# Performance work log

Measured on AMD Instinct MI355X. Metric: run time of the kernel, lower is better.

The kernel has to match this reference:

```python
import jax, jax.numpy as jnp
import numpy as np

D_MODEL = 1024
N_HEADS = 16
D_K = D_MODEL // N_HEADS
SEQ = 2048
BATCH = 2
THETA = 10000.0


def apply_rope(x, positions, theta):
    # x: [..., h, s, d_k], positions: [s]
    d_k = x.shape[-1]
    inv_freq = 1.0 / (theta ** (jnp.arange(0, d_k, 2, dtype=jnp.float32) / d_k))  # [d_k/2]
    ang = positions.astype(jnp.float32)[:, None] * inv_freq[None, :]  # [s, d_k/2]
    cos, sin = jnp.cos(ang), jnp.sin(ang)
    xe, xo = x[..., 0::2], x[..., 1::2]
    re = xe * cos - xo * sin
    ro = xe * sin + xo * cos
    return jnp.stack([re, ro], axis=-1).reshape(x.shape)


def setup_inputs() -> dict:
    key = jax.random.key(0)
    ks = jax.random.split(key, 7)
    f = lambda k, s: jax.random.normal(k, s, dtype=jnp.float32)
    return {
        "Q": f(ks[0], (BATCH, SEQ, D_MODEL)),
        "K": f(ks[1], (BATCH, SEQ, D_MODEL)),
        "V": f(ks[2], (BATCH, SEQ, D_MODEL)),
        "w_q": f(ks[3], (D_MODEL, D_MODEL)) * 0.02,
        "w_k": f(ks[4], (D_MODEL, D_MODEL)) * 0.02,
        "w_v": f(ks[5], (D_MODEL, D_MODEL)) * 0.02,
        "w_o": f(ks[6], (D_MODEL, D_MODEL)) * 0.02,
        "mask": jnp.tril(jnp.ones((SEQ, SEQ), dtype=bool)),
        "token_positions": jnp.arange(SEQ, dtype=jnp.int32),
    }


def reference(Q, K, V, w_q, w_k, w_v, w_o, mask, token_positions):
    h, d_k = N_HEADS, D_K
    # projections: weight is [h*d_k, d_model], applied as x @ W^T
    def proj(x, w):
        y = jnp.einsum('bsd,ed->bse', x, w)
        b, s, _ = y.shape
        return y.reshape(b, s, h, d_k).transpose(0, 2, 1, 3)  # [b,h,s,d_k]
    q = proj(Q, w_q)
    k = proj(K, w_k)
    v = proj(V, w_v)
    q = apply_rope(q, token_positions, THETA)
    k = apply_rope(k, token_positions, THETA)
    scores = jnp.einsum('bhqd,bhkd->bhqk', q, k) / jnp.sqrt(jnp.float32(d_k))
    scores = jnp.where(mask, scores, -jnp.inf)
    attn = jax.nn.softmax(scores, axis=-1)
    out = jnp.einsum('bhqk,bhkd->bhqd', attn, v)
    b, _, s, _ = out.shape
    out = out.transpose(0, 2, 1, 3).reshape(b, s, h * d_k)
    return jnp.einsum('bse,de->bsd', out, w_o)
```

## Files before the change

### kernel.cpp

```cpp
#include <hip/hip_runtime.h>

#define SEQ 2048
#define BATCH 2
#define DM 1024
#define NH 16
#define DK 64
#define BH (BATCH*NH)

typedef __attribute__((ext_vector_type(8))) short bf16x8;
typedef __attribute__((ext_vector_type(4))) float f32x4;

__device__ __forceinline__ ushort f2bf(float f) {
  union { float f; unsigned u; } v; v.f = f;
  unsigned r = (v.u + 0x7fffu + ((v.u >> 16) & 1u)) >> 16;
  return (ushort)r;
}
__device__ __forceinline__ float bf2f(ushort h) {
  union { unsigned u; float f; } v; v.u = ((unsigned)h) << 16;
  return v.f;
}
__device__ __forceinline__ unsigned cvtpk(float lo, float hi) {
  unsigned r;
  asm("v_cvt_pk_bf16_f32 %0, %1, %2" : "=v"(r) : "v"(lo), "v"(hi));
  return r;
}

struct P4 { const float* p0; const float* p1; const float* p2; const float* p3; };
__global__ void k_castN(P4 in, ushort* __restrict__ out, int n4) {
  const float* src = (blockIdx.z == 0) ? in.p0 : (blockIdx.z == 1) ? in.p1
                    : (blockIdx.z == 2) ? in.p2 : in.p3;
  ushort* dst = out + (size_t)blockIdx.z * (size_t)n4 * 4;
  int i = blockIdx.x * blockDim.x + threadIdx.x;
  int st = gridDim.x * blockDim.x;
  for (; i < n4; i += st) {
    float4 v = reinterpret_cast<const float4*>(src)[i];
    ushort4 o;
    o.x = f2bf(v.x); o.y = f2bf(v.y); o.z = f2bf(v.z); o.w = f2bf(v.w);
    reinterpret_cast<ushort4*>(dst)[i] = o;
  }
}

__global__ void k_rope_tab(float* __restrict__ tab) {
  int id = blockIdx.x * blockDim.x + threadIdx.x;
  if (id >= SEQ * 32) return;
  int s = id >> 5, i = id & 31;
  float inv = powf(10000.f, -(float)i / 32.f);
  float ang = (float)s * inv;
  float sn, cs;
  sincosf(ang, &sn, &cs);
  tab[id * 2] = cs;
  tab[id * 2 + 1] = sn;
}

__global__ __launch_bounds__(256) void k_tr_v(const ushort* __restrict__ Y,
                                              ushort* __restrict__ VT) {
  __shared__ ushort tile[64][65];
  const int st = blockIdx.x, bh = blockIdx.y;
  const int b = bh >> 4, h = bh & 15;
  const int d = threadIdx.x & 63, s4 = threadIdx.x >> 6;
#pragma unroll
  for (int p = 0; p < 16; ++p) {
    int sl = p * 4 + s4;
    tile[d][sl] = Y[(size_t)(b * SEQ + st * 64 + sl) * DM + h * 64 + d];
  }
  __syncthreads();
  const int sl = threadIdx.x & 63, d4 = threadIdx.x >> 6;
#pragma unroll
  for (int p = 0; p < 16; ++p) {
    int dl = p * 4 + d4;
    VT[(size_t)bh * DK * SEQ + (size_t)dl * SEQ + st * 64 + sl] = tile[dl][sl];
  }
}

__device__ __forceinline__ void gll16(const void* g, void* l) {
  __builtin_amdgcn_global_load_lds((const __attribute__((address_space(1))) void*)g,
                                   (__attribute__((address_space(3))) void*)l, 16, 0, 0);
}

#define GSTAGE(AD, BD, kk_) do {                                               \
    gll16(A + (size_t)(m0 + w * 16 + lrow) * K + (kk_) + lcol, (void*)((AD) + w * 512));        \
    gll16(A + (size_t)(m0 + 64 + w * 16 + lrow) * K + (kk_) + lcol, (void*)((AD) + 2048 + w * 512)); \
    gll16(Bw + (size_t)(n0 + w * 16 + lrow) * K + (kk_) + lcol, (void*)((BD) + w * 512));       \
    gll16(Bw + (size_t)(n0 + 64 + w * 16 + lrow) * K + (kk_) + lcol, (void*)((BD) + 2048 + w * 512)); \
  } while (0)

#define GCOMP(AS_, BS_) do {                                                   \
    bf16x8 af[4], bfr[4];                                                      \
    _Pragma("unroll")                                                          \
    for (int i = 0; i < 4; ++i)                                                \
      af[i] = *(const bf16x8*)((AS_) + (wr * 64 + i * 16 + l15) * 32 + l4 * 8);\
    _Pragma("unroll")                                                          \
    for (int i = 0; i < 4; ++i)                                                \
      bfr[i] = *(const bf16x8*)((BS_) + (wc * 64 + i * 16 + l15) * 32 + l4 * 8);\
    _Pragma("unroll")                                                          \
    for (int mi = 0; mi < 4; ++mi)                                             \
      _Pragma("unroll")                                                        \
      for (int ni = 0; ni < 4; ++ni)                                           \
        acc[mi][ni] = __builtin_amdgcn_mfma_f32_16x16x32_bf16(af[mi], bfr[ni], acc[mi][ni], 0, 0, 0); \
  } while (0)

__global__ __launch_bounds__(256) void k_gemm_qkv(const ushort* __restrict__ A,
                                                  const ushort* __restrict__ Bw,
                                                  ushort* __restrict__ qT,
                                                  ushort* __restrict__ kT,
                                                  ushort* __restrict__ YV,
                                                  const float* __restrict__ tab,
                                                  float qscale, int M, int N, int K) {
  const int z = blockIdx.z;
  A += (size_t)z * ((size_t)M * K);
  Bw += (size_t)z * ((size_t)N * K);
  __shared__ ushort As0[128 * 32], Bs0[128 * 32];
  __shared__ ushort As1[128 * 32], Bs1[128 * 32];
  const int tid = threadIdx.x;
  const int w = tid >> 6, lane = tid & 63;
  const int l15 = lane & 15, l4 = lane >> 4;
  const int m0 = blockIdx.y * 128, n0 = blockIdx.x * 128;
  const int wr = w >> 1, wc = w & 1;
  const int lrow = lane >> 2, lcol = (lane & 3) * 8;
  f32x4 acc[4][4] = {};
  GSTAGE(As0, Bs0, 0);
  __syncthreads();
  for (int kk = 0; kk < K; kk += 64) {
    GSTAGE(As1, Bs1, kk + 32);
    GCOMP(As0, Bs0);
    __syncthreads();
    if (kk + 64 < K) GSTAGE(As0, Bs0, kk + 64);
    GCOMP(As1, Bs1);
    __syncthreads();
  }
  if (z == 2) {
#pragma unroll
    for (int mi = 0; mi < 4; ++mi)
#pragma unroll
      for (int ni = 0; ni < 4; ++ni)
#pragma unroll
        for (int r = 0; r < 4; ++r) {
          int row = m0 + wr * 64 + mi * 16 + l4 * 4 + r;
          int col = n0 + wc * 64 + ni * 16 + l15;
          YV[(size_t)row * N + col] = f2bf(acc[mi][ni][r]);
        }
  } else {
    const float scale = (z == 0) ? qscale : 1.0f;
    ushort* T = (z == 0) ? qT : kT;
    const bool odd = (l15 & 1);
#pragma unroll
    for (int mi = 0; mi < 4; ++mi)
#pragma unroll
      for (int ni = 0; ni < 4; ++ni)
#pragma unroll
        for (int r = 0; r < 4; ++r) {
          int row = m0 + wr * 64 + mi * 16 + l4 * 4 + r;
          int col = n0 + wc * 64 + ni * 16 + l15;
          float v = acc[mi][ni][r];
          float pv = __shfl_xor(v, 1);
          int s = row & (SEQ - 1);
          int d = col & 63;
          float2 cs = *(const float2*)(tab + ((size_t)s * 32 + (d >> 1)) * 2);
          float xe = odd ? pv : v, xo = odd ? v : pv;
          float outv = (odd ? (xe * cs.y + xo * cs.x) : (xe * cs.x - xo * cs.y)) * scale;
          int bh = (row >> 11) * 16 + (col >> 6);
          T[((size_t)bh * SEQ + s) * 64 + d] = f2bf(outv);
        }
  }
}

#define FSTAGE(AD, BD, kk_) do {                                               \
    gll16(A + (size_t)(m0 + srow) * K + (kk_) + scol, (void*)((AD) + w * 512));\
    gll16(Bw + (size_t)(n0 + srow) * K + (kk_) + scol, (void*)((BD) + w * 512));\
    gll16(Bw + (size_t)(n0 + 64 + srow) * K + (kk_) + scol, (void*)((BD) + 2048 + w * 512)); \
  } while (0)

#define FCOMP(AS_, BS_) do {                                                   \
    bf16x8 af[2], bfr[4];                                                      \
    _Pragma("unroll")                                                          \
    for (int i = 0; i < 2; ++i)                                                \
      af[i] = *(const bf16x8*)((AS_) + (wr * 32 + i * 16 + l15) * 32 + l4 * 8);\
    _Pragma("unroll")                                                          \
    for (int i = 0; i < 4; ++i)                                                \
      bfr[i] = *(const bf16x8*)((BS_) + (wc * 64 + i * 16 + l15) * 32 + l4 * 8);\
    _Pragma("unroll")                                                          \
    for (int mi = 0; mi < 2; ++mi)                                             \
      _Pragma("unroll")                                                        \
      for (int ni = 0; ni < 4; ++ni)                                           \
        acc[mi][ni] = __builtin_amdgcn_mfma_f32_16x16x32_bf16(af[mi], bfr[ni], acc[mi][ni], 0, 0, 0); \
  } while (0)

__global__ __launch_bounds__(256) void k_gemm_f(const ushort* __restrict__ A,
                                                const ushort* __restrict__ Bw,
                                                float* __restrict__ C, int M, int N, int K) {
  __shared__ ushort As0[64 * 32], Bs0[128 * 32];
  __shared__ ushort As1[64 * 32], Bs1[128 * 32];
  const int tid = threadIdx.x;
  const int w = tid >> 6, lane = tid & 63;
  const int l15 = lane & 15, l4 = lane >> 4;
  const int m0 = blockIdx.y * 64, n0 = blockIdx.x * 128;
  const int wr = w >> 1, wc = w & 1;
  const int srow = tid >> 2, scol = (tid & 3) * 8;
  f32x4 acc[2][4] = {};
  FSTAGE(As0, Bs0, 0);
  __syncthreads();
  for (int kk = 0; kk < K; kk += 64) {
    FSTAGE(As1, Bs1, kk + 32);
    FCOMP(As0, Bs0);
    __syncthreads();
    if (kk + 64 < K) FSTAGE(As0, Bs0, kk + 64);
    FCOMP(As1, Bs1);
    __syncthreads();
  }
#pragma unroll
  for (int mi = 0; mi < 2; ++mi)
#pragma unroll
    for (int ni = 0; ni < 4; ++ni)
#pragma unroll
      for (int r = 0; r < 4; ++r) {
        int row = m0 + wr * 32 + mi * 16 + l4 * 4 + r;
        int col = n0 + wc * 64 + ni * 16 + l15;
        C[(size_t)row * N + col] = acc[mi][ni][r];
      }
}

#define STAGE1(DST, src, srcstride) do {                                       \
    _Pragma("unroll")                                                          \
    for (int i_ = 0; i_ < 2; ++i_) {                                           \
      int tt_ = i_ * 256 + tid;                                                \
      int row_ = tt_ >> 3, c_ = (tt_ & 7) ^ (row_ & 7);                        \
      gll16(src + (size_t)row_ * (srcstride) + c_ * 8,                         \
            (void*)((char*)(DST) + (i_ * 256 + w * 64) * 16));                 \
    }                                                                          \
  } while (0)

#define STAGE(KD, VD, kt_) do {                                                \
    const ushort* kb_ = kT + hb + (size_t)(kt_) * 4096;                        \
    const ushort* vb_ = vT + vbase + (size_t)(kt_) * 64;                       \
    STAGE1(KD, kb_, 64);                                                       \
    STAGE1(VD, vb_, SEQ);                                                      \
  } while (0)

#define LDSFRAG(BASE, row_, cidx)                                              \
  (*(const bf16x8*)((const char*)(BASE) + (row_) * 128 + (((cidx) ^ (l15 & 7)) * 16)))

#define SMAXUPD(P, MRUN, LRUN, SO) do {                                        \
    float a0 = fmaxf(fmaxf(P[0][0], P[0][1]), fmaxf(P[0][2], P[0][3]));        \
    float a1 = fmaxf(fmaxf(P[1][0], P[1][1]), fmaxf(P[1][2], P[1][3]));        \
    float a2 = fmaxf(fmaxf(P[2][0], P[2][1]), fmaxf(P[2][2], P[2][3]));        \
    float a3 = fmaxf(fmaxf(P[3][0], P[3][1]), fmaxf(P[3][2], P[3][3]));        \
    float mx = fmaxf(fmaxf(a0, a1), fmaxf(a2, a3));                            \
    mx = fmaxf(mx, __shfl_xor(mx, 16));                                        \
    mx = fmaxf(mx, __shfl_xor(mx, 32));                                        \
    const float mn = fmaxf(MRUN, mx);                                          \
    SO = __builtin_amdgcn_exp2f(MRUN - mn);                                    \
    float rs = 0.f;                                                            \
    _Pragma("unroll")                                                          \
    for (int nf = 0; nf < 4; ++nf) {                                           \
      float e0 = __builtin_amdgcn_exp2f(P[nf][0] - mn);                        \
      float e1 = __builtin_amdgcn_exp2f(P[nf][1] - mn);                        \
      float e2 = __builtin_amdgcn_exp2f(P[nf][2] - mn);                        \
      float e3 = __builtin_amdgcn_exp2f(P[nf][3] - mn);                        \
      P[nf][0] = e0; P[nf][1] = e1; P[nf][2] = e2; P[nf][3] = e3;              \
      rs += (e0 + e1) + (e2 + e3);                                             \
    }                                                                          \
    rs += __shfl_xor(rs, 16);                                                  \
    rs += __shfl_xor(rs, 32);                                                  \
    LRUN = LRUN * SO + rs;                                                     \
    MRUN = mn;                                                                 \
  } while (0)

#define RESCALE(ACC, SO) do {                                                  \
    float soq[4];                                                              \
    _Pragma("unroll")                                                          \
    for (int r = 0; r < 4; ++r) soq[r] = __shfl(SO, l4 * 4 + r);               \
    _Pragma("unroll")                                                          \
    for (int df = 0; df < 4; ++df)                                             \
      _Pragma("unroll")                                                        \
      for (int r = 0; r < 4; ++r) ACC[df][r] *= soq[r];                        \
  } while (0)

#define PWRITE(P, MYP) do {                                                    \
    _Pragma("unroll")                                                          \
    for (int nf = 0; nf < 4; ++nf) {                                           \
      uint2 pk;                                                                \
      pk.x = cvtpk(P[nf][0], P[nf][1]);                                        \
      pk.y = cvtpk(P[nf][2], P[nf][3]);                                        \
      *(uint2*)((MYP) + ((l15 * 128 + nf * 32 + l4 * 8) ^ swz)) = pk;          \
    }                                                                          \
  } while (0)

#define STEP2(KC, VC, KN, VN, kt_, M0, M1, PREF) do {                          \
    if (PREF) { STAGE(KN, VN, (kt_) + 1); }                                    \
    float p0[4][4], p1[4][4];                                                  \
    _Pragma("unroll")                                                          \
    for (int nf = 0; nf < 4; ++nf) {                                           \
      bf16x8 k0_ = LDSFRAG(KC, nf * 16 + l15, l4);                             \
      bf16x8 k1_ = LDSFRAG(KC, nf * 16 + l15, l4 + 4);                         \
      if (M0 >= 0) {                                                           \
        f32x4 z = {0.f, 0.f, 0.f, 0.f};                                        \
        z = __builtin_amdgcn_mfma_f32_16x16x32_bf16(k0_, qb00, z, 0, 0, 0);    \
        z = __builtin_amdgcn_mfma_f32_16x16x32_bf16(k1_, qb01, z, 0, 0, 0);    \
        _Pragma("unroll")                                                      \
        for (int r = 0; r < 4; ++r) {                                          \
          float sc = z[r];                                                     \
          if (M0 == 1 && (nf * 16 + l4 * 4 + r) > (w * 16 + l15)) sc = -INFINITY; \
          p0[nf][r] = sc;                                                      \
        }                                                                      \
      }                                                                        \
      {                                                                        \
        f32x4 z = {0.f, 0.f, 0.f, 0.f};                                        \
        z = __builtin_amdgcn_mfma_f32_16x16x32_bf16(k0_, qb10, z, 0, 0, 0);    \
        z = __builtin_amdgcn_mfma_f32_16x16x32_bf16(k1_, qb11, z, 0, 0, 0);    \
        _Pragma("unroll")                                                      \
        for (int r = 0; r < 4; ++r) {                                          \
          float sc = z[r];                                                     \
          if (M1 == 1 && (nf * 16 + l4 * 4 + r) > (w * 16 + l15)) sc = -INFINITY; \
          p1[nf][r] = sc;                                                      \
        }                                                                      \
      }                                                                        \
    }                                                                          \
    float so0_, so1_;                                                          \
    if (M0 >= 0) { SMAXUPD(p0, mrun0, lrun0, so0_); RESCALE(acc0, so0_); PWRITE(p0, myP0); } \
    SMAXUPD(p1, mrun1, lrun1, so1_); RESCALE(acc1, so1_); PWRITE(p1, myP1);    \
    bf16x8 pa00, pa01, pa10, pa11;                                             \
    if (M0 >= 0) {                                                             \
      pa00 = *(const bf16x8*)(myP0 + ((l15 * 128 + l4 * 16) ^ swz));           \
      pa01 = *(const bf16x8*)(myP0 + ((l15 * 128 + 64 + l4 * 16) ^ swz));      \
    }                                                                          \
    pa10 = *(const bf16x8*)(myP1 + ((l15 * 128 + l4 * 16) ^ swz));             \
    pa11 = *(const bf16x8*)(myP1 + ((l15 * 128 + 64 + l4 * 16) ^ swz));        \
    _Pragma("unroll")                                                          \
    for (int df = 0; df < 4; ++df) {                                           \
      bf16x8 v0_ = LDSFRAG(VC, df * 16 + l15, l4);                             \
      bf16x8 v1_ = LDSFRAG(VC, df * 16 + l15, l4 + 4);                         \
      if (M0 >= 0) {                                                           \
        acc0[df] = __builtin_amdgcn_mfma_f32_16x16x32_bf16(pa00, v0_, acc0[df], 0, 0, 0); \
        acc0[df] = __builtin_amdgcn_mfma_f32_16x16x32_bf16(pa01, v1_, acc0[df], 0, 0, 0); \
      }                                                                        \
      acc1[df] = __builtin_amdgcn_mfma_f32_16x16x32_bf16(pa10, v0_, acc1[df], 0, 0, 0); \
      acc1[df] = __builtin_amdgcn_mfma_f32_16x16x32_bf16(pa11, v1_, acc1[df], 0, 0, 0); \
    }                                                                          \
    __syncthreads();                                                           \
  } while (0)

__global__ __launch_bounds__(256, 3) void k_flash(const ushort* __restrict__ qT,
                                                  const ushort* __restrict__ kT,
                                                  const ushort* __restrict__ vT,
                                                  ushort* __restrict__ AO) {
  __shared__ ushort Ks[2][64 * 64];
  __shared__ ushort Vs[2][64 * 64];
  __shared__ char Plds[4 * 4096];
  const int l = blockIdx.x;
  const int bh = (l & 7) * 4 + ((l >> 3) & 3);
  const int qt = (SEQ / 128 - 1) - (l >> 5);
  const int tid = threadIdx.x, w = tid >> 6, lane = tid & 63;
  const int l15 = lane & 15, l4 = lane >> 4;
  const size_t hb = (size_t)bh * SEQ * DK;
  const size_t vbase = (size_t)bh * DK * SEQ;
  const int qrow0 = qt * 128 + w * 16;
  const int qrow1 = qrow0 + 64;
  const bf16x8 qb00 = *(const bf16x8*)(qT + hb + (size_t)(qrow0 + l15) * 64 + l4 * 8);
  const bf16x8 qb01 = *(const bf16x8*)(qT + hb + (size_t)(qrow0 + l15) * 64 + 32 + l4 * 8);
  const bf16x8 qb10 = *(const bf16x8*)(qT + hb + (size_t)(qrow1 + l15) * 64 + l4 * 8);
  const bf16x8 qb11 = *(const bf16x8*)(qT + hb + (size_t)(qrow1 + l15) * 64 + 32 + l4 * 8);
  f32x4 acc0[4] = {}, acc1[4] = {};
  float mrun0 = -INFINITY, lrun0 = 0.f, mrun1 = -INFINITY, lrun1 = 0.f;
  char* myP0 = (char*)Plds + w * 4096;
  char* myP1 = myP0 + 2048;
  const int swz = (l15 & 7) << 4;
  ushort* kc = &Ks[0][0]; ushort* vc = &Vs[0][0];
  ushort* kn = &Ks[1][0]; ushort* vn = &Vs[1][0];
  STAGE(kc, vc, 0);
  __syncthreads();
  for (int kt = 0; kt < 2 * qt; ++kt) {
    STEP2(kc, vc, kn, vn, kt, 0, 0, true);
    ushort* t;
    t = kc; kc = kn; kn = t;
    t = vc; vc = vn; vn = t;
  }
  STEP2(kc, vc, kn, vn, 2 * qt, 1, 0, true);
  {
    ushort* t;
    t = kc; kc = kn; kn = t;
    t = vc; vc = vn; vn = t;
  }
  STEP2(kc, vc, kn, vn, 2 * qt + 1, -1, 1, false);
  const int b = bh >> 4, h = bh & 15;
  float lq0[4], lq1[4];
#pragma unroll
  for (int r = 0; r < 4; ++r) {
    lq0[r] = __shfl(lrun0, l4 * 4 + r);
    lq1[r] = __shfl(lrun1, l4 * 4 + r);
  }
#pragma unroll
  for (int r = 0; r < 4; ++r) {
    float inv0 = 1.f / lq0[r], inv1 = 1.f / lq1[r];
    int qr0 = qrow0 + l4 * 4 + r, qr1 = qrow1 + l4 * 4 + r;
#pragma unroll
    for (int df = 0; df < 4; ++df) {
      AO[(size_t)(b * SEQ + qr0) * DM + h * 64 + df * 16 + l15] = f2bf(acc0[df][r] * inv0);
      AO[(size_t)(b * SEQ + qr1) * DM + h * 64 + df * 16 + l15] = f2bf(acc1[df][r] * inv1);
    }
  }
}

extern "C" void kernel_launch(void* const* d_in, const int* in_sizes, int n_in,
                              void* d_out, int out_size, void* d_ws, size_t ws_size,
                              hipStream_t stream) {
  const float* Q = (const float*)d_in[0];
  const float* K = (const float*)d_in[1];
  const float* V = (const float*)d_in[2];
  const float* wq = (const float*)d_in[3];
  const float* wk = (const float*)d_in[4];
  const float* wv = (const float*)d_in[5];
  const float* wo = (const float*)d_in[6];
  float* out = (float*)d_out;
  char* ws = (char*)d_ws;

  ushort* XQ = (ushort*)(ws + 0);
  ushort* XK = (ushort*)(ws + 8388608);
  ushort* WQ = (ushort*)(ws + 25165824);
  ushort* qT = (ushort*)(ws + 33554432);
  ushort* kT = (ushort*)(ws + 41943040);
  ushort* YV = (ushort*)(ws + 50331648);
  float* TAB = (float*)(ws + 58720256);
  ushort* vT = XQ;
  ushort* AO = XK;

  const int NX4 = BATCH * SEQ * DM / 4;
  const int NW4 = DM * DM / 4;
  P4 xin = {Q, K, V, nullptr};
  P4 win = {wq, wk, wv, wo};
  k_castN<<<dim3(1024, 1, 3), 256, 0, stream>>>(xin, XQ, NX4);
  k_castN<<<dim3(1024, 1, 4), 256, 0, stream>>>(win, WQ, NW4);
  k_rope_tab<<<(SEQ * 32) / 256, 256, 0, stream>>>(TAB);

  const float QSCALE = 0.125f * 1.4426950408889634f;
  k_gemm_qkv<<<dim3(DM / 128, (BATCH * SEQ) / 128, 3), 256, 0, stream>>>(
      XQ, WQ, qT, kT, YV, TAB, QSCALE, BATCH * SEQ, DM, DM);

  k_tr_v<<<dim3(SEQ / 64, BH), 256, 0, stream>>>(YV, vT);

  k_flash<<<BH * (SEQ / 128), 256, 0, stream>>>(qT, kT, vT, AO);

  k_gemm_f<<<dim3(DM / 128, (BATCH * SEQ) / 64), 256, 0, stream>>>(
      AO, WQ + 3 * DM * DM, out, BATCH * SEQ, DM, DM);
}
```

Measured before the change: 140.9 us.

## Deepen GEMM prefetch with explicit vmcnt waits and swizzle block order

Rewrites the QKV and output-projection GEMM main loops so two K-stages are in flight. It uses explicit s_waitcnt vmcnt/lgkmcnt plus raw barriers in place of __syncthreads, letting the next global-to-LDS load overlap compute instead of waiting on every load. It also flattens the grid to 1D and remaps block IDs into 8x8 M/N groups to improve L2 reuse of A and B tiles. The hand-set vmcnt thresholds depend on exactly how many loads each stage issues, so miscounting could cause races.

```diff
diff --git a/kernel.cpp b/kernel.cpp
--- a/kernel.cpp
+++ b/kernel.cpp
@@ -24,6 +24,12 @@
   asm("v_cvt_pk_bf16_f32 %0, %1, %2" : "=v"(r) : "v"(lo), "v"(hi));
   return r;
 }
+
+#define WAITV4 asm volatile("s_waitcnt vmcnt(4)" ::: "memory")
+#define WAITV3 asm volatile("s_waitcnt vmcnt(3)" ::: "memory")
+#define WAITV0 asm volatile("s_waitcnt vmcnt(0)" ::: "memory")
+#define WAITL0 asm volatile("s_waitcnt lgkmcnt(0)" ::: "memory")
+#define BARR() __builtin_amdgcn_s_barrier()
 
 struct P4 { const float* p0; const float* p1; const float* p2; const float* p3; };
 __global__ void k_castN(P4 in, ushort* __restrict__ out, int n4) {
@@ -106,7 +112,9 @@
                                                   ushort* __restrict__ YV,
                                                   const float* __restrict__ tab,
                                                   float qscale, int M, int N, int K) {
-  const int z = blockIdx.z;
+  const int id = blockIdx.x;
+  const int mlo = id & 7, nb = (id >> 3) & 7, mhi = (id >> 6) & 3, z = id >> 8;
+  const int m0 = (mhi * 8 + mlo) * 128, n0 = nb * 128;
   A += (size_t)z * ((size_t)M * K);
   Bw += (size_t)z * ((size_t)N * K);
   __shared__ ushort As0[128 * 32], Bs0[128 * 32];
@@ -114,20 +122,25 @@
   const int tid = threadIdx.x;
   const int w = tid >> 6, lane = tid & 63;
   const int l15 = lane & 15, l4 = lane >> 4;
-  const int m0 = blockIdx.y * 128, n0 = blockIdx.x * 128;
   const int wr = w >> 1, wc = w & 1;
   const int lrow = lane >> 2, lcol = (lane & 3) * 8;
   f32x4 acc[4][4] = {};
   GSTAGE(As0, Bs0, 0);
-  __syncthreads();
-  for (int kk = 0; kk < K; kk += 64) {
-    GSTAGE(As1, Bs1, kk + 32);
+  GSTAGE(As1, Bs1, 32);
+  for (int kk = 0; kk < K - 64; kk += 64) {
+    WAITV4; BARR();
     GCOMP(As0, Bs0);
-    __syncthreads();
-    if (kk + 64 < K) GSTAGE(As0, Bs0, kk + 64);
+    WAITL0; BARR();
+    GSTAGE(As0, Bs0, kk + 64);
+    WAITV4; BARR();
     GCOMP(As1, Bs1);
-    __syncthreads();
-  }
+    WAITL0; BARR();
+    if (kk + 96 < K) GSTAGE(As1, Bs1, kk + 96);
+  }
+  WAITV4; BARR();
+  GCOMP(As0, Bs0);
+  WAITV0; BARR();
+  GCOMP(As1, Bs1);
   if (z == 2) {
 #pragma unroll
     for (int mi = 0; mi < 4; ++mi)
@@ -188,25 +201,33 @@
 __global__ __launch_bounds__(256) void k_gemm_f(const ushort* __restrict__ A,
                                                 const ushort* __restrict__ Bw,
                                                 float* __restrict__ C, int M, int N, int K) {
+  const int id = blockIdx.x;
+  const int mlo = id & 7, nb = (id >> 3) & 7, mhi = id >> 6;
+  const int m0 = (mhi * 8 + mlo) * 64, n0 = nb * 128;
   __shared__ ushort As0[64 * 32], Bs0[128 * 32];
   __shared__ ushort As1[64 * 32], Bs1[128 * 32];
   const int tid = threadIdx.x;
   const int w = tid >> 6, lane = tid & 63;
   const int l15 = lane & 15, l4 = lane >> 4;
-  const int m0 = blockIdx.y * 64, n0 = blockIdx.x * 128;
   const int wr = w >> 1, wc = w & 1;
   const int srow = tid >> 2, scol = (tid & 3) * 8;
   f32x4 acc[2][4] = {};
   FSTAGE(As0, Bs0, 0);
-  __syncthreads();
-  for (int kk = 0; kk < K; kk += 64) {
-    FSTAGE(As1, Bs1, kk + 32);
+  FSTAGE(As1, Bs1, 32);
+  for (int kk = 0; kk < K - 64; kk += 64) {
+    WAITV3; BARR();
     FCOMP(As0, Bs0);
-    __syncthreads();
-    if (kk + 64 < K) FSTAGE(As0, Bs0, kk + 64);
+    WAITL0; BARR();
+    FSTAGE(As0, Bs0, kk + 64);
+    WAITV3; BARR();
     FCOMP(As1, Bs1);
-    __syncthreads();
-  }
+    WAITL0; BARR();
+    if (kk + 96 < K) FSTAGE(As1, Bs1, kk + 96);
+  }
+  WAITV3; BARR();
+  FCOMP(As0, Bs0);
+  WAITV0; BARR();
+  FCOMP(As1, Bs1);
 #pragma unroll
   for (int mi = 0; mi < 2; ++mi)
 #pragma unroll
@@ -432,13 +453,12 @@
   k_rope_tab<<<(SEQ * 32) / 256, 256, 0, stream>>>(TAB);
 
   const float QSCALE = 0.125f * 1.4426950408889634f;
-  k_gemm_qkv<<<dim3(DM / 128, (BATCH * SEQ) / 128, 3), 256, 0, stream>>>(
-      XQ, WQ, qT, kT, YV, TAB, QSCALE, BATCH * SEQ, DM, DM);
+  k_gemm_qkv<<<768, 256, 0, stream>>>(XQ, WQ, qT, kT, YV, TAB, QSCALE,
+                                      BATCH * SEQ, DM, DM);
 
   k_tr_v<<<dim3(SEQ / 64, BH), 256, 0, stream>>>(YV, vT);
 
   k_flash<<<BH * (SEQ / 128), 256, 0, stream>>>(qT, kT, vT, AO);
 
-  k_gemm_f<<<dim3(DM / 128, (BATCH * SEQ) / 64), 256, 0, stream>>>(
-      AO, WQ + 3 * DM * DM, out, BATCH * SEQ, DM, DM);
-}
+  k_gemm_f<<<512, 256, 0, stream>>>(AO, WQ + 3 * DM * DM, out, BATCH * SEQ, DM, DM);
+}
```

After: 130.2 us. 7.6% less time.
